# Kernel tuning notes

Hardware: AMD Instinct MI355X
Metric: run time of the kernel (lower is better)

The kernel has to match this reference:

```python
import jax, jax.numpy as jnp
import numpy as np

N_C, N_T, N_D = 50000, 30000, 20000
N = N_C + N_T + N_D
R = 4          # num relations
E_R = 400000   # edges per relation (contiguous blocks in edge_index)
L = 2          # num layers
H = 256        # hidden dim
EPS = 1e-5


def _layernorm(x, g, b):
    mu = jnp.mean(x, axis=-1, keepdims=True)
    var = jnp.mean(jnp.square(x - mu), axis=-1, keepdims=True)
    return (x - mu) * jax.lax.rsqrt(var + EPS) * g + b


def setup_inputs() -> dict:
    key = jax.random.key(0)
    ks = jax.random.split(key, 16)
    s = 0.02
    return {
        "x_compound": jax.random.normal(ks[0], (N_C, 256), jnp.float32),
        "x_target": jax.random.normal(ks[1], (N_T, 512), jnp.float32),
        "x_disease": jax.random.normal(ks[2], (N_D, 128), jnp.float32),
        "edge_index": jax.random.randint(ks[3], (2, R * E_R), 0, N, jnp.int32),
        "Wp_compound": jax.random.normal(ks[4], (256, H), jnp.float32) * s,
        "bp_compound": jnp.zeros((H,), jnp.float32),
        "Wp_target": jax.random.normal(ks[5], (512, H), jnp.float32) * s,
        "bp_target": jnp.zeros((H,), jnp.float32),
        "Wp_disease": jax.random.normal(ks[6], (128, H), jnp.float32) * s,
        "bp_disease": jnp.zeros((H,), jnp.float32),
        "rgcn_w": jax.random.normal(ks[7], (L, R, H, H), jnp.float32) * s,
        "rgcn_root": jax.random.normal(ks[8], (L, H, H), jnp.float32) * s,
        "rgcn_b": jnp.zeros((L, H), jnp.float32),
        "ln_g": jnp.ones((L, H), jnp.float32),
        "ln_b": jnp.zeros((L, H), jnp.float32),
        "Wo": jax.random.normal(ks[9], (H, H), jnp.float32) * s,
        "bo": jnp.zeros((H,), jnp.float32),
    }


def reference(x_compound, x_target, x_disease, edge_index,
              Wp_compound, bp_compound, Wp_target, bp_target,
              Wp_disease, bp_disease, rgcn_w, rgcn_root, rgcn_b,
              ln_g, ln_b, Wo, bo):
    # input projections per entity type, then concat (dict -> combined tensor)
    h = jnp.concatenate([
        x_compound @ Wp_compound + bp_compound,
        x_target @ Wp_target + bp_target,
        x_disease @ Wp_disease + bp_disease,
    ], axis=0)  # [N, H]

    for l in range(L):
        # RGCNConv (num_bases=None, aggr='add'): root transform + per-relation scatter-add
        out = h @ rgcn_root[l] + rgcn_b[l]
        for r in range(R):
            src = edge_index[0, r * E_R:(r + 1) * E_R]
            dst = edge_index[1, r * E_R:(r + 1) * E_R]
            msg = (h @ rgcn_w[l, r])[src]                 # [E_R, H] gather
            out = out + jax.ops.segment_sum(msg, dst, num_segments=N)
        if l > 0:  # residual only for layer_idx > 0
            out = out + h
        out = _layernorm(out, ln_g[l], ln_b[l])
        # dropout is identity in eval mode
        h = out

    y = h @ Wo + bo
    return (y[:N_C], y[N_C:N_C + N_T], y[N_C + N_T:])
```

## Files before the change

kernel.cpp:

```cpp
#include <hip/hip_runtime.h>
#include <hip/hip_bf16.h>

namespace {
constexpr int kNC = 50000;
constexpr int kNT = 30000;
constexpr int kND = 20000;
constexpr int kN  = 100000;
constexpr int kR  = 4;
constexpr int kER = 400000;
constexpr int kE  = kR * kER;
constexpr int kH  = 256;
constexpr int kB  = kR * kN;

constexpr int padM(int m) { return (m + 127) / 128 * 128; }
}

typedef __attribute__((ext_vector_type(8))) short short8;
typedef __attribute__((ext_vector_type(4))) float f32x4;
typedef __attribute__((ext_vector_type(4))) unsigned short us4;

__device__ __forceinline__ unsigned short f2bf(float x) {
    unsigned u = __builtin_bit_cast(unsigned, x);
    u += 0x7FFF + ((u >> 16) & 1);
    return (unsigned short)(u >> 16);
}
__device__ __forceinline__ float bf2f(unsigned short u) {
    unsigned v = ((unsigned)u) << 16;
    return __builtin_bit_cast(float, v);
}
__device__ __forceinline__ float bf2f_s(short u) {
    unsigned v = ((unsigned)(unsigned short)u) << 16;
    return __builtin_bit_cast(float, v);
}

__device__ __forceinline__ void gld16(const void* src, void* lds) {
    __builtin_amdgcn_global_load_lds(
        (const __attribute__((address_space(1))) void*)src,
        (__attribute__((address_space(3))) void*)lds, 16, 0, 0);
}

__device__ __forceinline__ void nt_store_f(float* p, float v) {
    __builtin_nontemporal_store(v, p);
}

__global__ __launch_bounds__(256)
void gemm_mfma(const unsigned short* __restrict__ A, int lda,
               const unsigned short* __restrict__ Bt, int ldb,
               const float* __restrict__ bias,
               float* __restrict__ Cf, unsigned short* __restrict__ Cb,
               int M, int K, int accumulate)
{
    __shared__ __attribute__((aligned(16))) unsigned short As[128 * 32];
    __shared__ __attribute__((aligned(16))) unsigned short Bs[128 * 32];
    const int tid  = threadIdx.x;
    const int lane = tid & 63;
    const int wid  = tid >> 6;
    const int wm   = wid >> 1;
    const int wn   = wid & 1;
    const int row0 = blockIdx.y * 128;
    const int col0 = blockIdx.x * 128;

    const int cr = lane >> 2;
    const int cs = lane & 3;

    const f32x4 z4 = {0.f, 0.f, 0.f, 0.f};
    f32x4 acc[4][4];
    #pragma unroll
    for (int m = 0; m < 4; ++m)
        #pragma unroll
        for (int n = 0; n < 4; ++n) acc[m][n] = z4;

    const int fr = lane & 15;
    const int kb = lane >> 4;

    for (int k0 = 0; k0 < K; k0 += 32) {
        #pragma unroll
        for (int j = 0; j < 2; ++j) {
            const int chunk = wid * 2 + j;
            const int r  = chunk * 16 + cr;
            const int sg = cs ^ ((r >> 1) & 3);
            gld16(A  + (size_t)(row0 + r) * lda + k0 + sg * 8, As + chunk * 512);
            gld16(Bt + (size_t)(col0 + r) * ldb + k0 + sg * 8, Bs + chunk * 512);
        }
        __syncthreads();
        short8 a[4], b[4];
        #pragma unroll
        for (int m = 0; m < 4; ++m) {
            const int am = wm * 64 + m * 16 + fr;
            const int s  = kb ^ ((am >> 1) & 3);
            a[m] = *(const short8*)(As + am * 32 + s * 8);
        }
        #pragma unroll
        for (int n = 0; n < 4; ++n) {
            const int bn = wn * 64 + n * 16 + fr;
            const int s  = kb ^ ((bn >> 1) & 3);
            b[n] = *(const short8*)(Bs + bn * 32 + s * 8);
        }
        #pragma unroll
        for (int m = 0; m < 4; ++m)
            #pragma unroll
            for (int n = 0; n < 4; ++n)
                acc[m][n] = __builtin_amdgcn_mfma_f32_16x16x32_bf16(
                    a[m], b[n], acc[m][n], 0, 0, 0);
        __syncthreads();
    }

    const int fq = lane >> 4;
    #pragma unroll
    for (int m = 0; m < 4; ++m) {
        #pragma unroll
        for (int n = 0; n < 4; ++n) {
            const int col  = col0 + wn * 64 + n * 16 + fr;
            const int rowb = row0 + wm * 64 + m * 16 + fq * 4;
            const float bv = bias ? bias[col] : 0.0f;
            #pragma unroll
            for (int i = 0; i < 4; ++i) {
                const int row = rowb + i;
                if (row >= M) continue;
                const float v = acc[m][n][i] + bv;
                const size_t idx = (size_t)row * kH + col;
                if (Cb) Cb[idx] = f2bf(v);
                else if (accumulate) Cf[idx] += v;
                else nt_store_f(&Cf[idx], v);
            }
        }
    }
}

__global__ __launch_bounds__(512, 2)
void rgcn_fused(const unsigned short* __restrict__ h_cur,
                const int* __restrict__ off, const int* __restrict__ esort,
                const unsigned short* __restrict__ W2,
                const float* __restrict__ bias, const float* __restrict__ g,
                const float* __restrict__ b,
                unsigned short* __restrict__ h_nxt, int useResid)
{
    __shared__ __attribute__((aligned(16))) unsigned short A_rel[4][32 * 256];
    __shared__ __attribute__((aligned(16))) unsigned short A_root[32 * 256];
    float (*red)[8][32] = reinterpret_cast<float (*)[8][32]>(A_rel);

    const int tid  = threadIdx.x;
    const int lane = tid & 63;
    const int wid  = tid >> 6;
    const int wcol = wid;
    const int rel  = wid & 3;
    const int rhalf= wid >> 2;
    const int row0 = blockIdx.x * 32;
    const int fr   = lane & 15;
    const int kb   = lane >> 4;
    const int eg   = lane >> 4;
    const int sl   = lane & 15;

    const f32x4 z4 = {0.f, 0.f, 0.f, 0.f};
    f32x4 acc[2][2];
    #pragma unroll
    for (int m = 0; m < 2; ++m)
        #pragma unroll
        for (int n = 0; n < 2; ++n) acc[m][n] = z4;

    {
        char* const rBase = reinterpret_cast<char*>(A_root);
        #pragma unroll
        for (int i = 0; i < 2; ++i) {
            const int base = wid * 2048 + i * 1024;
            const int o = base + lane * 16;
            const int row = o >> 9;
            const int offr = (o & 511) ^ ((row & 7) << 4);
            gld16(h_cur + (size_t)(row0 + row) * kH + (offr >> 1), rBase + base);
        }
    }

    {
        char* const aBase = reinterpret_cast<char*>(A_rel[rel]);
        int offv = 0;
        if (lane < 17) offv = off[(size_t)rel * kN + row0 + rhalf * 16 + lane];
        #pragma unroll
        for (int batch = 0; batch < 4; ++batch) {
            const int wrow = rhalf * 16 + batch * 4 + eg;
            const int t0 = __shfl(offv, batch * 4 + eg);
            const int t1 = __shfl(offv, batch * 4 + eg + 1);
            float a[16];
            #pragma unroll
            for (int i = 0; i < 16; ++i) a[i] = 0.f;
            int t = t0;
            for (; t + 2 <= t1; t += 2) {
                const int s0 = esort[t];
                const int s1 = esort[t + 1];
                const short8 v0a = *reinterpret_cast<const short8*>(
                    h_cur + (size_t)s0 * kH + sl * 16);
                const short8 v0b = *reinterpret_cast<const short8*>(
                    h_cur + (size_t)s0 * kH + sl * 16 + 8);
                const short8 v1a = *reinterpret_cast<const short8*>(
                    h_cur + (size_t)s1 * kH + sl * 16);
                const short8 v1b = *reinterpret_cast<const short8*>(
                    h_cur + (size_t)s1 * kH + sl * 16 + 8);
                #pragma unroll
                for (int i = 0; i < 8; ++i) {
                    a[i]     += bf2f_s(v0a[i]) + bf2f_s(v1a[i]);
                    a[8 + i] += bf2f_s(v0b[i]) + bf2f_s(v1b[i]);
                }
            }
            if (t < t1) {
                const int s0 = esort[t];
                const short8 v0a = *reinterpret_cast<const short8*>(
                    h_cur + (size_t)s0 * kH + sl * 16);
                const short8 v0b = *reinterpret_cast<const short8*>(
                    h_cur + (size_t)s0 * kH + sl * 16 + 8);
                #pragma unroll
                for (int i = 0; i < 8; ++i) {
                    a[i]     += bf2f_s(v0a[i]);
                    a[8 + i] += bf2f_s(v0b[i]);
                }
            }
            short8 w0, w1;
            #pragma unroll
            for (int i = 0; i < 8; ++i) {
                w0[i] = (short)f2bf(a[i]);
                w1[i] = (short)f2bf(a[8 + i]);
            }
            const int byte0 = (wrow * 512 + sl * 32) ^ ((wrow & 7) << 4);
            *reinterpret_cast<short8*>(aBase + byte0) = w0;
            *reinterpret_cast<short8*>(aBase + (byte0 ^ 16)) = w1;
        }
    }

    __syncthreads();

    for (int p = 0; p < 5; ++p) {
        char* const aBase = (p < 4) ? reinterpret_cast<char*>(A_rel[p])
                                    : reinterpret_cast<char*>(A_root);
        const unsigned short* Wp = W2 + (size_t)p * 8 * 8192;
        #pragma unroll
        for (int ks = 0; ks < 8; ++ks) {
            const unsigned short* Wks = Wp + ks * 8192;
            const int kByte = ks * 64 + kb * 16;
            short8 a[2], bf[2];
            #pragma unroll
            for (int m = 0; m < 2; ++m) {
                const int am = m * 16 + fr;
                const int byte = (am * 512 + kByte) ^ ((am & 7) << 4);
                a[m] = *reinterpret_cast<const short8*>(aBase + byte);
            }
            #pragma unroll
            for (int n = 0; n < 2; ++n) {
                const int cn = wcol * 32 + n * 16 + fr;
                bf[n] = *reinterpret_cast<const short8*>(Wks + cn * 32 + kb * 8);
            }
            #pragma unroll
            for (int m = 0; m < 2; ++m)
                #pragma unroll
                for (int n = 0; n < 2; ++n)
                    acc[m][n] = __builtin_amdgcn_mfma_f32_16x16x32_bf16(
                        a[m], bf[n], acc[m][n], 0, 0, 0);
        }
    }

    __syncthreads();

    const int fq = lane >> 4;
    #pragma unroll
    for (int m = 0; m < 2; ++m) {
        #pragma unroll
        for (int i = 0; i < 4; ++i) {
            const int rowloc = m * 16 + fq * 4 + i;
            const int row = row0 + rowloc;
            float s = 0.f, q = 0.f;
            #pragma unroll
            for (int n = 0; n < 2; ++n) {
                const int col = wcol * 32 + n * 16 + fr;
                float v = acc[m][n][i] + bias[col];
                if (useResid) v += bf2f(h_cur[(size_t)row * kH + col]);
                acc[m][n][i] = v;
                s += v;
                q += v * v;
            }
            #pragma unroll
            for (int w = 1; w <= 8; w <<= 1) {
                s += __shfl_xor(s, w);
                q += __shfl_xor(q, w);
            }
            if (fr == 0) { red[0][wcol][rowloc] = s; red[1][wcol][rowloc] = q; }
        }
    }
    __syncthreads();
    #pragma unroll
    for (int m = 0; m < 2; ++m) {
        #pragma unroll
        for (int i = 0; i < 4; ++i) {
            const int rowloc = m * 16 + fq * 4 + i;
            const int row = row0 + rowloc;
            float s = 0.f, qq = 0.f;
            #pragma unroll
            for (int w = 0; w < 8; ++w) {
                s  += red[0][w][rowloc];
                qq += red[1][w][rowloc];
            }
            const float mu = s * (1.0f / kH);
            const float var = qq * (1.0f / kH) - mu * mu;
            const float rstd = rsqrtf(var + 1e-5f);
            #pragma unroll
            for (int n = 0; n < 2; ++n) {
                const int col = wcol * 32 + n * 16 + fr;
                const float o = (acc[m][n][i] - mu) * rstd * g[col] + b[col];
                h_nxt[(size_t)row * kH + col] = f2bf(o);
            }
        }
    }
}


__global__ __launch_bounds__(256)
void conv_bf16(const float* __restrict__ in, unsigned short* __restrict__ out, int n)
{
    int i = (blockIdx.x * 256 + threadIdx.x) * 4;
    if (i >= n) return;
    f32x4 v = *reinterpret_cast<const f32x4*>(in + i);
    us4 o = { f2bf(v.x), f2bf(v.y), f2bf(v.z), f2bf(v.w) };
    *reinterpret_cast<us4*>(out + i) = o;
}

__global__ __launch_bounds__(256)
void wT_bf16(const float* __restrict__ W, unsigned short* __restrict__ Wt, int K)
{
    int t = blockIdx.x * 256 + threadIdx.x;
    if (t >= 256 * K) return;
    int c = t / K, k = t % K;
    Wt[t] = f2bf(W[(size_t)k * 256 + c]);
}

__global__ __launch_bounds__(256)
void wstack2_bf16(const float* __restrict__ w, const float* __restrict__ root,
                  unsigned short* __restrict__ W2)
{
    int t = blockIdx.x * 256 + threadIdx.x;
    if (t >= 5 * 8 * 256 * 32) return;
    const int e   = t & 7;
    const int kb  = (t >> 3) & 3;
    const int col = (t >> 5) & 255;
    const int ks  = (t >> 13) & 7;
    const int p   = t >> 16;
    const int k   = p * 256 + ks * 32 + kb * 8 + e;
    const float v = (k < 1024) ? w[(size_t)k * 256 + col]
                               : root[(size_t)(k - 1024) * 256 + col];
    W2[t] = f2bf(v);
}


__global__ __launch_bounds__(256)
void count_deg(const int* __restrict__ dst, int* __restrict__ deg, int nE)
{
    int e = blockIdx.x * 256 + threadIdx.x;
    if (e >= nE) return;
    int r = e / kER;
    atomicAdd(&deg[r * kN + dst[e]], 1);
}

__global__ __launch_bounds__(256)
void chunk_reduce(const int* __restrict__ deg, int* __restrict__ chunkSum, int B)
{
    __shared__ int sm[256];
    int s = 0;
    #pragma unroll
    for (int j = 0; j < 4; ++j) {
        int idx = blockIdx.x * 1024 + j * 256 + threadIdx.x;
        if (idx < B) s += deg[idx];
    }
    sm[threadIdx.x] = s;
    __syncthreads();
    for (int o = 128; o >= 1; o >>= 1) {
        if (threadIdx.x < o) sm[threadIdx.x] += sm[threadIdx.x + o];
        __syncthreads();
    }
    if (threadIdx.x == 0) chunkSum[blockIdx.x] = sm[0];
}

__global__ __launch_bounds__(64)
void scan_chunks(const int* __restrict__ chunkSum, int* __restrict__ chunkBase, int n)
{
    int lane = threadIdx.x;
    int base = 0;
    for (int i0 = 0; i0 < n; i0 += 64) {
        int i = i0 + lane;
        int orig = (i < n) ? chunkSum[i] : 0;
        int v = orig;
        #pragma unroll
        for (int o = 1; o < 64; o <<= 1) {
            int t = __shfl_up(v, o);
            if (lane >= o) v += t;
        }
        if (i < n) chunkBase[i] = base + v - orig;
        base += __shfl(v, 63);
    }
}

__global__ __launch_bounds__(256)
void scan_within(const int* __restrict__ deg, const int* __restrict__ chunkBase,
                 int* __restrict__ off, int B)
{
    __shared__ int ts[256];
    const int i0 = blockIdx.x * 1024;
    int v[4];
    int s = 0;
    #pragma unroll
    for (int j = 0; j < 4; ++j) {
        int idx = i0 + threadIdx.x * 4 + j;
        v[j] = (idx < B) ? deg[idx] : 0;
        s += v[j];
    }
    ts[threadIdx.x] = s;
    __syncthreads();
    for (int o = 1; o < 256; o <<= 1) {
        int u = (threadIdx.x >= o) ? ts[threadIdx.x - o] : 0;
        __syncthreads();
        ts[threadIdx.x] += u;
        __syncthreads();
    }
    int run = chunkBase[blockIdx.x] + ts[threadIdx.x] - s;
    #pragma unroll
    for (int j = 0; j < 4; ++j) {
        int idx = i0 + threadIdx.x * 4 + j;
        if (idx <= B) off[idx] = run;
        run += v[j];
    }
}

__global__ __launch_bounds__(256)
void fill_csr(const int* __restrict__ src, const int* __restrict__ dst,
              int* __restrict__ cursor, int* __restrict__ esort, int nE)
{
    int e = blockIdx.x * 256 + threadIdx.x;
    if (e >= nE) return;
    int r = e / kER;
    int pos = atomicAdd(&cursor[r * kN + dst[e]], 1);
    esort[pos] = src[e];
}


extern "C" void kernel_launch(void* const* d_in, const int* in_sizes, int n_in,
                              void* d_out, int out_size, void* d_ws, size_t ws_size,
                              hipStream_t stream)
{
    const float* x_c  = (const float*)d_in[0];
    const float* x_t  = (const float*)d_in[1];
    const float* x_d  = (const float*)d_in[2];
    const int*   ei   = (const int*)d_in[3];
    const float* Wp_c = (const float*)d_in[4];
    const float* bp_c = (const float*)d_in[5];
    const float* Wp_t = (const float*)d_in[6];
    const float* bp_t = (const float*)d_in[7];
    const float* Wp_d = (const float*)d_in[8];
    const float* bp_d = (const float*)d_in[9];
    const float* rgcn_w    = (const float*)d_in[10];
    const float* rgcn_root = (const float*)d_in[11];
    const float* rgcn_b    = (const float*)d_in[12];
    const float* ln_g = (const float*)d_in[13];
    const float* ln_b = (const float*)d_in[14];
    const float* Wo   = (const float*)d_in[15];
    const float* bo   = (const float*)d_in[16];

    const int* src_base = ei;
    const int* dst_base = ei + (size_t)kE;

    const int nChunks = (kB + 1023) / 1024;
    const int pN  = padM(kN);
    const int pNC = padM(kNC);
    const int pNT = padM(kNT);
    const int pND = padM(kND);

    char* p = (char*)d_ws;
    unsigned short* hA = (unsigned short*)p;  p += (size_t)pN * kH * 2;
    unsigned short* hB = (unsigned short*)p;  p += (size_t)pN * kH * 2;
    unsigned short* xbf_c = (unsigned short*)p;  p += (size_t)pNC * 256 * 2;
    unsigned short* xbf_t = (unsigned short*)p;  p += (size_t)pNT * 512 * 2;
    unsigned short* xbf_d = (unsigned short*)p;  p += (size_t)pND * 128 * 2;
    unsigned short* Wt_c = (unsigned short*)p;
    unsigned short* Wt_t = Wt_c + 256 * 256;
    unsigned short* Wt_d = Wt_t + 256 * 512;
    unsigned short* W2   = Wt_d + 256 * 128;
    unsigned short* Wt_o = W2 + 2 * 5 * 8 * 256 * 32;
    p = (char*)(Wt_o + 256 * 256);

    int* deg    = (int*)p;
    int* off    = deg + kB;
    int* esort  = off + (kB + 1);
    int* chunkS = esort + kE;
    int* chunkB = chunkS + 1024;

    float* outf = (float*)d_out;

    const dim3 blk(256);

    hipMemsetAsync(deg, 0, (size_t)kB * sizeof(int), stream);
    count_deg<<<dim3((kE + 255) / 256), blk, 0, stream>>>(dst_base, deg, kE);
    chunk_reduce<<<dim3(nChunks), blk, 0, stream>>>(deg, chunkS, kB);
    scan_chunks<<<dim3(1), dim3(64), 0, stream>>>(chunkS, chunkB, nChunks);
    scan_within<<<dim3(nChunks), blk, 0, stream>>>(deg, chunkB, off, kB);
    hipMemcpyAsync(deg, off, (size_t)kB * sizeof(int), hipMemcpyDeviceToDevice, stream);
    fill_csr<<<dim3((kE + 255) / 256), blk, 0, stream>>>(src_base, dst_base, deg, esort, kE);

    conv_bf16<<<dim3((kNC * 256 / 4 + 255) / 256), blk, 0, stream>>>(x_c, xbf_c, kNC * 256);
    conv_bf16<<<dim3((kNT * 512 / 4 + 255) / 256), blk, 0, stream>>>(x_t, xbf_t, kNT * 512);
    conv_bf16<<<dim3((kND * 128 / 4 + 255) / 256), blk, 0, stream>>>(x_d, xbf_d, kND * 128);
    wT_bf16<<<dim3((256 * 256 + 255) / 256), blk, 0, stream>>>(Wp_c, Wt_c, 256);
    wT_bf16<<<dim3((256 * 512 + 255) / 256), blk, 0, stream>>>(Wp_t, Wt_t, 512);
    wT_bf16<<<dim3((256 * 128 + 255) / 256), blk, 0, stream>>>(Wp_d, Wt_d, 128);
    wT_bf16<<<dim3((256 * 256 + 255) / 256), blk, 0, stream>>>(Wo, Wt_o, 256);
    for (int l = 0; l < 2; ++l)
        wstack2_bf16<<<dim3(5 * 8 * 256 * 32 / 256), blk, 0, stream>>>(
            rgcn_w + (size_t)l * kR * kH * kH, rgcn_root + (size_t)l * kH * kH,
            W2 + (size_t)l * 5 * 8 * 256 * 32);

    gemm_mfma<<<dim3(2, pNC / 128), blk, 0, stream>>>(
        xbf_c, 256, Wt_c, 256, bp_c, nullptr, hA, kNC, 256, 0);
    gemm_mfma<<<dim3(2, pNT / 128), blk, 0, stream>>>(
        xbf_t, 512, Wt_t, 512, bp_t, nullptr, hA + (size_t)kNC * kH, kNT, 512, 0);
    gemm_mfma<<<dim3(2, pND / 128), blk, 0, stream>>>(
        xbf_d, 128, Wt_d, 128, bp_d, nullptr, hA + (size_t)(kNC + kNT) * kH, kND, 128, 0);

    const dim3 fusedGrid(kN / 32);
    const dim3 fusedBlk(512);
    rgcn_fused<<<fusedGrid, fusedBlk, 0, stream>>>(
        hA, off, esort, W2, rgcn_b, ln_g, ln_b, hB, 0);
    rgcn_fused<<<fusedGrid, fusedBlk, 0, stream>>>(
        hB, off, esort, W2 + (size_t)5 * 8 * 256 * 32,
        rgcn_b + kH, ln_g + kH, ln_b + kH, hA, 1);

    gemm_mfma<<<dim3(2, pN / 128), blk, 0, stream>>>(
        hA, 256, Wt_o, 256, bo, outf, nullptr, kN, 256, 0);
}
```

Baseline: 904.5 us.

## Reuse one LDS tile per relation and interleave gather with MFMA phases

Shared memory is cut from five 16KB tiles to a single 16KB tile. The kernel now loops over relations: all waves cooperatively gather and aggregate one relation's neighbour sum into the tile, then run that relation's MFMA pass before moving to the next relation, with the root tile loaded last. The gather is also restructured so each lane holds 8 channels and the edge loop is unrolled by four for more memory-level parallelism. The intent is higher occupancy from the smaller LDS footprint and better latency hiding. The cost is extra barriers per block and serialization between gather and compute inside a block.

```diff
diff --git a/kernel.cpp b/kernel.cpp
--- a/kernel.cpp
+++ b/kernel.cpp
@@ -135,21 +135,19 @@
                 const float* __restrict__ b,
                 unsigned short* __restrict__ h_nxt, int useResid)
 {
-    __shared__ __attribute__((aligned(16))) unsigned short A_rel[4][32 * 256];
-    __shared__ __attribute__((aligned(16))) unsigned short A_root[32 * 256];
-    float (*red)[8][32] = reinterpret_cast<float (*)[8][32]>(A_rel);
+    __shared__ __attribute__((aligned(16))) unsigned short A_seg[32 * 256];
+    __shared__ float red[2][8][32];
 
     const int tid  = threadIdx.x;
     const int lane = tid & 63;
     const int wid  = tid >> 6;
-    const int wcol = wid;
-    const int rel  = wid & 3;
-    const int rhalf= wid >> 2;
     const int row0 = blockIdx.x * 32;
     const int fr   = lane & 15;
     const int kb   = lane >> 4;
     const int eg   = lane >> 4;
     const int sl   = lane & 15;
+    const int grow = eg >> 1;
+    const int ghalf= eg & 1;
 
     const f32x4 z4 = {0.f, 0.f, 0.f, 0.f};
     f32x4 acc[2][2];
@@ -158,77 +156,62 @@
         #pragma unroll
         for (int n = 0; n < 2; ++n) acc[m][n] = z4;
 
-    {
-        char* const rBase = reinterpret_cast<char*>(A_root);
-        #pragma unroll
-        for (int i = 0; i < 2; ++i) {
-            const int base = wid * 2048 + i * 1024;
-            const int o = base + lane * 16;
-            const int row = o >> 9;
-            const int offr = (o & 511) ^ ((row & 7) << 4);
-            gld16(h_cur + (size_t)(row0 + row) * kH + (offr >> 1), rBase + base);
-        }
-    }
-
-    {
-        char* const aBase = reinterpret_cast<char*>(A_rel[rel]);
-        int offv = 0;
-        if (lane < 17) offv = off[(size_t)rel * kN + row0 + rhalf * 16 + lane];
-        #pragma unroll
-        for (int batch = 0; batch < 4; ++batch) {
-            const int wrow = rhalf * 16 + batch * 4 + eg;
-            const int t0 = __shfl(offv, batch * 4 + eg);
-            const int t1 = __shfl(offv, batch * 4 + eg + 1);
-            float a[16];
-            #pragma unroll
-            for (int i = 0; i < 16; ++i) a[i] = 0.f;
-            int t = t0;
-            for (; t + 2 <= t1; t += 2) {
-                const int s0 = esort[t];
-                const int s1 = esort[t + 1];
-                const short8 v0a = *reinterpret_cast<const short8*>(
-                    h_cur + (size_t)s0 * kH + sl * 16);
-                const short8 v0b = *reinterpret_cast<const short8*>(
-                    h_cur + (size_t)s0 * kH + sl * 16 + 8);
-                const short8 v1a = *reinterpret_cast<const short8*>(
-                    h_cur + (size_t)s1 * kH + sl * 16);
-                const short8 v1b = *reinterpret_cast<const short8*>(
-                    h_cur + (size_t)s1 * kH + sl * 16 + 8);
+    char* const aBase = reinterpret_cast<char*>(A_seg);
+
+    for (int p = 0; p < 5; ++p) {
+        __syncthreads();
+        if (p < 4) {
+            int offv = 0;
+            if (lane < 5) offv = off[(size_t)p * kN + row0 + wid * 4 + lane];
+            #pragma unroll
+            for (int batch = 0; batch < 2; ++batch) {
+                const int wrow = wid * 4 + batch * 2 + grow;
+                const int t0 = __shfl(offv, batch * 2 + grow);
+                const int t1 = __shfl(offv, batch * 2 + grow + 1);
+                float a[8];
                 #pragma unroll
-                for (int i = 0; i < 8; ++i) {
-                    a[i]     += bf2f_s(v0a[i]) + bf2f_s(v1a[i]);
-                    a[8 + i] += bf2f_s(v0b[i]) + bf2f_s(v1b[i]);
+                for (int i = 0; i < 8; ++i) a[i] = 0.f;
+                const unsigned short* hp = h_cur + ghalf * 128 + sl * 8;
+                int t = t0;
+                for (; t + 4 <= t1; t += 4) {
+                    const int s0 = esort[t];
+                    const int s1 = esort[t + 1];
+                    const int s2 = esort[t + 2];
+                    const int s3 = esort[t + 3];
+                    const short8 v0 = *reinterpret_cast<const short8*>(hp + (size_t)s0 * kH);
+                    const short8 v1 = *reinterpret_cast<const short8*>(hp + (size_t)s1 * kH);
+                    const short8 v2 = *reinterpret_cast<const short8*>(hp + (size_t)s2 * kH);
+                    const short8 v3 = *reinterpret_cast<const short8*>(hp + (size_t)s3 * kH);
+                    #pragma unroll
+                    for (int i = 0; i < 8; ++i)
+                        a[i] += (bf2f_s(v0[i]) + bf2f_s(v1[i]))
+                              + (bf2f_s(v2[i]) + bf2f_s(v3[i]));
                 }
-            }
-            if (t < t1) {
-                const int s0 = esort[t];
-                const short8 v0a = *reinterpret_cast<const short8*>(
-                    h_cur + (size_t)s0 * kH + sl * 16);
-                const short8 v0b = *reinterpret_cast<const short8*>(
-                    h_cur + (size_t)s0 * kH + sl * 16 + 8);
+                for (; t < t1; ++t) {
+                    const int s0 = esort[t];
+                    const short8 v0 = *reinterpret_cast<const short8*>(hp + (size_t)s0 * kH);
+                    #pragma unroll
+                    for (int i = 0; i < 8; ++i) a[i] += bf2f_s(v0[i]);
+                }
+                short8 w0;
                 #pragma unroll
-                for (int i = 0; i < 8; ++i) {
-                    a[i]     += bf2f_s(v0a[i]);
-                    a[8 + i] += bf2f_s(v0b[i]);
-                }
-            }
-            short8 w0, w1;
-            #pragma unroll
-            for (int i = 0; i < 8; ++i) {
-                w0[i] = (short)f2bf(a[i]);
-                w1[i] = (short)f2bf(a[8 + i]);
-            }
-            const int byte0 = (wrow * 512 + sl * 32) ^ ((wrow & 7) << 4);
-            *reinterpret_cast<short8*>(aBase + byte0) = w0;
-            *reinterpret_cast<short8*>(aBase + (byte0 ^ 16)) = w1;
-        }
-    }
-
-    __syncthreads();
-
-    for (int p = 0; p < 5; ++p) {
-        char* const aBase = (p < 4) ? reinterpret_cast<char*>(A_rel[p])
-                                    : reinterpret_cast<char*>(A_root);
+                for (int i = 0; i < 8; ++i) w0[i] = (short)f2bf(a[i]);
+                const int byte0 = (wrow * 512 + ghalf * 256 + sl * 16)
+                                ^ ((wrow & 7) << 4);
+                *reinterpret_cast<short8*>(aBase + byte0) = w0;
+            }
+        } else {
+            #pragma unroll
+            for (int i = 0; i < 2; ++i) {
+                const int base = wid * 2048 + i * 1024;
+                const int o = base + lane * 16;
+                const int row = o >> 9;
+                const int offr = (o & 511) ^ ((row & 7) << 4);
+                gld16(h_cur + (size_t)(row0 + row) * kH + (offr >> 1), aBase + base);
+            }
+        }
+        __syncthreads();
+
         const unsigned short* Wp = W2 + (size_t)p * 8 * 8192;
         #pragma unroll
         for (int ks = 0; ks < 8; ++ks) {
@@ -243,7 +226,7 @@
             }
             #pragma unroll
             for (int n = 0; n < 2; ++n) {
-                const int cn = wcol * 32 + n * 16 + fr;
+                const int cn = wid * 32 + n * 16 + fr;
                 bf[n] = *reinterpret_cast<const short8*>(Wks + cn * 32 + kb * 8);
             }
             #pragma unroll
@@ -255,8 +238,6 @@
         }
     }
 
-    __syncthreads();
-
     const int fq = lane >> 4;
     #pragma unroll
     for (int m = 0; m < 2; ++m) {
@@ -267,7 +248,7 @@
             float s = 0.f, q = 0.f;
             #pragma unroll
             for (int n = 0; n < 2; ++n) {
-                const int col = wcol * 32 + n * 16 + fr;
+                const int col = wid * 32 + n * 16 + fr;
                 float v = acc[m][n][i] + bias[col];
                 if (useResid) v += bf2f(h_cur[(size_t)row * kH + col]);
                 acc[m][n][i] = v;
@@ -279,7 +260,7 @@
                 s += __shfl_xor(s, w);
                 q += __shfl_xor(q, w);
             }
-            if (fr == 0) { red[0][wcol][rowloc] = s; red[1][wcol][rowloc] = q; }
+            if (fr == 0) { red[0][wid][rowloc] = s; red[1][wid][rowloc] = q; }
         }
     }
     __syncthreads();
@@ -300,7 +281,7 @@
             const float rstd = rsqrtf(var + 1e-5f);
             #pragma unroll
             for (int n = 0; n < 2; ++n) {
-                const int col = wcol * 32 + n * 16 + fr;
+                const int col = wid * 32 + n * 16 + fr;
                 const float o = (acc[m][n][i] - mu) * rstd * g[col] + b[col];
                 h_nxt[(size_t)row * kH + col] = f2bf(o);
             }
```

Result: slower. 966.0 us (+6.8%).
